# Optimization experiments

Measured on AMD Instinct MI355X. Metric: run time of the kernel, lower is better.

The kernel has to match this reference:

```python
import jax, jax.numpy as jnp
import numpy as np

B, T, LE = 8, 128, 128
V, VEXT = 32000, 32100
D, H, DFF, MAXLEN = 512, 8, 2048, 512


def _ln(x, g, b, eps=1e-5):
    m = jnp.mean(x, axis=-1, keepdims=True)
    v = jnp.mean((x - m) ** 2, axis=-1, keepdims=True)
    return (x - m) / jnp.sqrt(v + eps) * g + b


def _mha(q_in, k_in, v_in, in_w, in_b, out_w, out_b, mask=None):
    # torch nn.MultiheadAttention (batch_first): packed in_proj [3D, D]
    d = q_in.shape[-1]
    dh = d // H
    wq, wk, wv = in_w[:d], in_w[d:2 * d], in_w[2 * d:]
    bq, bk, bv = in_b[:d], in_b[d:2 * d], in_b[2 * d:]
    q = q_in @ wq.T + bq
    k = k_in @ wk.T + bk
    v = v_in @ wv.T + bv
    def split(x):  # [B, L, D] -> [B, H, L, dh]
        b, l, _ = x.shape
        return x.reshape(b, l, H, dh).transpose(0, 2, 1, 3)
    q, k, v = split(q), split(k), split(v)
    scores = jnp.einsum('bhqd,bhkd->bhqk', q, k) / jnp.sqrt(jnp.asarray(dh, q.dtype))
    if mask is not None:
        scores = scores + mask  # broadcast [T, T] additive mask
    attn = jax.nn.softmax(scores, axis=-1)  # [B, H, Lq, Lk]
    out = jnp.einsum('bhqk,bhkd->bhqd', attn, v)
    b, _, lq, _ = out.shape
    out = out.transpose(0, 2, 1, 3).reshape(b, lq, d)
    return out @ out_w.T + out_b, attn


def setup_inputs() -> dict:
    key = jax.random.key(0)
    ks = jax.random.split(key, 16)
    s = 0.02
    p = lambda i, shape: jax.random.normal(ks[i], shape, jnp.float32) * s
    return {
        'trg_input_ids': jax.random.randint(ks[0], (B, T), 0, V),
        'emofused': jax.random.normal(ks[1], (B, LE, D), jnp.float32),
        'src_token_ids': jax.random.randint(ks[2], (B, LE), 0, VEXT),
        'extended_vocab_size': VEXT,
        'tok_emb': p(3, (V, D)),
        'pos_emb': p(4, (MAXLEN, D)),
        'sa_in_w': p(5, (3 * D, D)), 'sa_in_b': jnp.zeros(3 * D, jnp.float32),
        'sa_out_w': p(6, (D, D)), 'sa_out_b': jnp.zeros(D, jnp.float32),
        'ca_in_w': p(7, (3 * D, D)), 'ca_in_b': jnp.zeros(3 * D, jnp.float32),
        'ca_out_w': p(8, (D, D)), 'ca_out_b': jnp.zeros(D, jnp.float32),
        'w1': p(9, (DFF, D)), 'b1': jnp.zeros(DFF, jnp.float32),
        'w2': p(10, (D, DFF)), 'b2': jnp.zeros(D, jnp.float32),
        'n1_g': jnp.ones(D, jnp.float32), 'n1_b': jnp.zeros(D, jnp.float32),
        'n2_g': jnp.ones(D, jnp.float32), 'n2_b': jnp.zeros(D, jnp.float32),
        'n3_g': jnp.ones(D, jnp.float32), 'n3_b': jnp.zeros(D, jnp.float32),
        'vp_w': p(11, (V, D)), 'vp_b': jnp.zeros(V, jnp.float32),
        'pg_w': p(12, (1, 3 * D)), 'pg_b': jnp.zeros(1, jnp.float32),
    }


def reference(trg_input_ids, emofused, src_token_ids, extended_vocab_size,
              tok_emb, pos_emb, sa_in_w, sa_in_b, sa_out_w, sa_out_b,
              ca_in_w, ca_in_b, ca_out_w, ca_out_b, w1, b1, w2, b2,
              n1_g, n1_b, n2_g, n2_b, n3_g, n3_b, vp_w, vp_b, pg_w, pg_b):
    t = trg_input_ids.shape[1]
    emb = tok_emb[trg_input_ids]                      # [B, T, D]
    x = emb + pos_emb[:t][None]
    # causal additive mask [T, T]
    idx = jnp.arange(t)
    mask = jnp.where(idx[None, :] > idx[:, None], jnp.asarray(-1e9, x.dtype), 0.0)
    # pre-norm self-attn
    h = _ln(x, n1_g, n1_b)
    sa, _ = _mha(h, h, h, sa_in_w, sa_in_b, sa_out_w, sa_out_b, mask)
    x = x + sa
    # pre-norm cross-attn (emofused is sole KV)
    h = _ln(x, n2_g, n2_b)
    ca, ca_attn = _mha(h, emofused, emofused, ca_in_w, ca_in_b, ca_out_w, ca_out_b)
    x = x + ca
    # FFN
    h = _ln(x, n3_g, n3_b)
    x = x + (jax.nn.relu(h @ w1.T + b1) @ w2.T + b2)
    hidden = x
    attn_avg = ca_attn.mean(axis=1)                   # [B, T, LE]
    ctx = jnp.einsum('btl,bld->btd', attn_avg, emofused)
    Pgen = jax.nn.softmax(hidden @ vp_w.T + vp_b, axis=-1)  # [B, T, V]
    gate_in = jnp.concatenate([hidden, ctx, emb], axis=-1)
    p_mix = jax.nn.sigmoid(gate_in @ pg_w.T + pg_b)   # [B, T, 1]
    vext = int(extended_vocab_size)
    def scat(aw, src):  # aw [T, LE], src [LE] -> [T, Vext]
        return jnp.zeros((aw.shape[0], vext), aw.dtype).at[:, src].add(aw)
    Pcopy = jax.vmap(scat)(attn_avg, src_token_ids)   # [B, T, Vext]
    Pgen_ext = jnp.pad(Pgen, ((0, 0), (0, 0), (0, vext - Pgen.shape[-1])))
    Pw = p_mix * Pgen_ext + (1.0 - p_mix) * Pcopy
    return Pw, Pgen_ext, Pcopy, p_mix, hidden, attn_avg, ctx
```

## Files before the change

kernel.cpp:

```cpp
#include <hip/hip_runtime.h>
#include <hip/hip_bf16.h>

using bf16   = __hip_bfloat16;
using bf16x8 = __attribute__((ext_vector_type(8))) __bf16;
using f32x4  = __attribute__((ext_vector_type(4))) float;
using short8 = __attribute__((ext_vector_type(8))) short;

__device__ __forceinline__ unsigned short f2b(float x) {
  union { bf16 b; unsigned short u; } t; t.b = __float2bfloat16(x); return t.u;
}
__device__ __forceinline__ float b2f(unsigned short u) {
  union { unsigned int i; float f; } t; t.i = ((unsigned int)u) << 16; return t.f;
}
__device__ __forceinline__ void ntst4(float* p, float a, float b, float c, float d) {
  f32x4 v = {a, b, c, d};
  __builtin_nontemporal_store(v, (f32x4*)p);
}

typedef __attribute__((address_space(1))) const unsigned int* gas1_t;
typedef __attribute__((address_space(3))) unsigned int* las3_t;
__device__ __forceinline__ void gload16(const void* g, void* l) {
  __builtin_amdgcn_global_load_lds((gas1_t)g, (las3_t)l, 16, 0, 0);
}

__global__ __launch_bounds__(256) void k_cast_all(
    const float* __restrict__ vpsrc, bf16* __restrict__ vpdst,
    const float* __restrict__ s0, bf16* __restrict__ d0,
    const float* __restrict__ s1, bf16* __restrict__ d1,
    const float* __restrict__ s2, bf16* __restrict__ d2,
    const float* __restrict__ s3, bf16* __restrict__ d3,
    const float* __restrict__ s4, bf16* __restrict__ d4,
    const float* __restrict__ s5, bf16* __restrict__ d5,
    const float* __restrict__ s6, bf16* __restrict__ d6,
    float* __restrict__ rowsum) {
  int i = blockIdx.x * 256 + threadIdx.x;
  int str = gridDim.x * 256;
  for (; i < 5275904; i += str) {
    if (i < 4096000) {
      float4 v = ((const float4*)vpsrc)[i];
      ushort4 u; u.x = f2b(v.x); u.y = f2b(v.y); u.z = f2b(v.z); u.w = f2b(v.w);
      ((ushort4*)vpdst)[i] = u;
    } else if (i < 5275648) {
      int j = i - 4096000;
      const float* s; bf16* d; int off;
      if      (j <  196608) { s = s0; d = d0; off = j; }
      else if (j <  262144) { s = s1; d = d1; off = j - 196608; }
      else if (j <  458752) { s = s2; d = d2; off = j - 262144; }
      else if (j <  524288) { s = s3; d = d3; off = j - 458752; }
      else if (j <  786432) { s = s4; d = d4; off = j - 524288; }
      else if (j < 1048576) { s = s5; d = d5; off = j - 786432; }
      else                  { s = s6; d = d6; off = j - 1048576; }
      float4 v = ((const float4*)s)[off];
      ushort4 u; u.x = f2b(v.x); u.y = f2b(v.y); u.z = f2b(v.z); u.w = f2b(v.w);
      ((ushort4*)d)[off] = u;
    } else {
      float4 z = {0.f, 0.f, 0.f, 0.f};
      ((float4*)rowsum)[i - 5275648] = z;
    }
  }
}

__global__ __launch_bounds__(256) void k_embed_ln(const int* __restrict__ ids, const float* __restrict__ tok,
                                                  const float* __restrict__ pos, const float* __restrict__ g,
                                                  const float* __restrict__ bb, float* __restrict__ x,
                                                  float* __restrict__ emb, bf16* __restrict__ o) {
  int wid = threadIdx.x >> 6, lane = threadIdx.x & 63;
  int row = blockIdx.x * 4 + wid;
  int tt = row & 127;
  int id = ids[row];
  int d = lane * 8;
  float4 e0 = *(const float4*)&tok[(size_t)id * 512 + d];
  float4 e1 = *(const float4*)&tok[(size_t)id * 512 + d + 4];
  float4 p0 = *(const float4*)&pos[(size_t)tt * 512 + d];
  float4 p1 = *(const float4*)&pos[(size_t)tt * 512 + d + 4];
  *(float4*)&emb[(size_t)row * 512 + d]     = e0;
  *(float4*)&emb[(size_t)row * 512 + d + 4] = e1;
  float4 v0; v0.x = e0.x + p0.x; v0.y = e0.y + p0.y; v0.z = e0.z + p0.z; v0.w = e0.w + p0.w;
  float4 v1; v1.x = e1.x + p1.x; v1.y = e1.y + p1.y; v1.z = e1.z + p1.z; v1.w = e1.w + p1.w;
  *(float4*)&x[(size_t)row * 512 + d]     = v0;
  *(float4*)&x[(size_t)row * 512 + d + 4] = v1;
  float s = v0.x + v0.y + v0.z + v0.w + v1.x + v1.y + v1.z + v1.w;
  float q = v0.x*v0.x + v0.y*v0.y + v0.z*v0.z + v0.w*v0.w
          + v1.x*v1.x + v1.y*v1.y + v1.z*v1.z + v1.w*v1.w;
#pragma unroll
  for (int t = 32; t; t >>= 1) { s += __shfl_xor(s, t); q += __shfl_xor(q, t); }
  float mean = s * (1.f / 512.f);
  float var  = q * (1.f / 512.f) - mean * mean;
  float rstd = rsqrtf(var + 1e-5f);
  float4 g0 = *(const float4*)&g[d],  g1 = *(const float4*)&g[d + 4];
  float4 b0 = *(const float4*)&bb[d], b1 = *(const float4*)&bb[d + 4];
  short8 pk;
  pk[0] = (short)f2b((v0.x - mean) * rstd * g0.x + b0.x);
  pk[1] = (short)f2b((v0.y - mean) * rstd * g0.y + b0.y);
  pk[2] = (short)f2b((v0.z - mean) * rstd * g0.z + b0.z);
  pk[3] = (short)f2b((v0.w - mean) * rstd * g0.w + b0.w);
  pk[4] = (short)f2b((v1.x - mean) * rstd * g1.x + b1.x);
  pk[5] = (short)f2b((v1.y - mean) * rstd * g1.y + b1.y);
  pk[6] = (short)f2b((v1.z - mean) * rstd * g1.z + b1.z);
  pk[7] = (short)f2b((v1.w - mean) * rstd * g1.w + b1.w);
  *(short8*)&o[(size_t)row * 512 + d] = pk;
}

__global__ __launch_bounds__(256) void k_ln(const float* __restrict__ x, const float* __restrict__ g,
                                            const float* __restrict__ bb, bf16* __restrict__ o) {
  int wid = threadIdx.x >> 6, lane = threadIdx.x & 63;
  int row = blockIdx.x * 4 + wid;
  const float* xr = x + (size_t)row * 512;
  int d = lane * 8;
  float4 v0 = *(const float4*)&xr[d];
  float4 v1 = *(const float4*)&xr[d + 4];
  float s = v0.x + v0.y + v0.z + v0.w + v1.x + v1.y + v1.z + v1.w;
  float q = v0.x*v0.x + v0.y*v0.y + v0.z*v0.z + v0.w*v0.w
          + v1.x*v1.x + v1.y*v1.y + v1.z*v1.z + v1.w*v1.w;
#pragma unroll
  for (int t = 32; t; t >>= 1) { s += __shfl_xor(s, t); q += __shfl_xor(q, t); }
  float mean = s * (1.f / 512.f);
  float var  = q * (1.f / 512.f) - mean * mean;
  float rstd = rsqrtf(var + 1e-5f);
  float4 g0 = *(const float4*)&g[d],  g1 = *(const float4*)&g[d + 4];
  float4 b0 = *(const float4*)&bb[d], b1 = *(const float4*)&bb[d + 4];
  short8 pk;
  pk[0] = (short)f2b((v0.x - mean) * rstd * g0.x + b0.x);
  pk[1] = (short)f2b((v0.y - mean) * rstd * g0.y + b0.y);
  pk[2] = (short)f2b((v0.z - mean) * rstd * g0.z + b0.z);
  pk[3] = (short)f2b((v0.w - mean) * rstd * g0.w + b0.w);
  pk[4] = (short)f2b((v1.x - mean) * rstd * g1.x + b1.x);
  pk[5] = (short)f2b((v1.y - mean) * rstd * g1.y + b1.y);
  pk[6] = (short)f2b((v1.z - mean) * rstd * g1.z + b1.z);
  pk[7] = (short)f2b((v1.w - mean) * rstd * g1.w + b1.w);
  *(short8*)&o[(size_t)row * 512 + d] = pk;
}

template<int RELU, int RESID, int OUTBF, int SWZ, int HID, int EXPS>
__global__ __launch_bounds__(256) void k_gemm(const bf16* __restrict__ A, const bf16* __restrict__ Wt,
                                              const float* __restrict__ bias, const float* __restrict__ resid,
                                              void* __restrict__ Cout, bf16* __restrict__ hidb,
                                              float* __restrict__ rowsum, int K, int ldc) {
  __shared__ __align__(16) float cst[32 * 132];
  bf16* Al = (bf16*)cst;
  bf16* Bl = (bf16*)cst + 4096;
  int t = threadIdx.x;
  int lane = t & 63;
  int wid = t >> 6;
  int wr = wid >> 1, wc = wid & 1;
  int trow, tcol;
  if (SWZ) {
    int bid = blockIdx.y * gridDim.x + blockIdx.x;
    int swz = (bid & 7) * 250 + (bid >> 3);
    trow = (swz & 7) * 128;
    tcol = (swz >> 3) * 128;
  } else {
    trow = blockIdx.y * 128; tcol = blockIdx.x * 128;
  }
  f32x4 acc[4][4] = {};
  const int kh = (lane >> 4) * 8;
  const int rl = lane & 15;
  const int srow = lane >> 2;
  const int scol = (lane & 3) * 8;
  for (int kt = 0; kt < K; kt += 32) {
    __syncthreads();
#pragma unroll
    for (int s = 0; s < 2; ++s) {
      int c = wid * 2 + s;
      int row = c * 16 + srow;
      gload16(A  + (size_t)(trow + row) * K + kt + scol, &Al[c * 512]);
      gload16(Wt + (size_t)(tcol + row) * K + kt + scol, &Bl[c * 512]);
    }
    __syncthreads();
    bf16x8 af[4], bg[4];
#pragma unroll
    for (int m = 0; m < 4; ++m) af[m] = *(const bf16x8*)&Al[(wr * 64 + m * 16 + rl) * 32 + kh];
#pragma unroll
    for (int n = 0; n < 4; ++n) bg[n] = *(const bf16x8*)&Bl[(wc * 64 + n * 16 + rl) * 32 + kh];
#pragma unroll
    for (int m = 0; m < 4; ++m)
#pragma unroll
      for (int n = 0; n < 4; ++n)
        acc[m][n] = __builtin_amdgcn_mfma_f32_16x16x32_bf16(af[m], bg[n], acc[m][n], 0, 0, 0);
  }
  const int s   = t >> 3;
  const int seg = (t & 7) * 16;
  float bv[16];
#pragma unroll
  for (int q = 0; q < 16; q += 4) *(float4*)&bv[q] = *(const float4*)&bias[tcol + seg + q];
#pragma unroll
  for (int m = 0; m < 4; ++m) {
    __syncthreads();
#pragma unroll
    for (int n = 0; n < 4; ++n) {
      int col = wc * 64 + n * 16 + rl;
#pragma unroll
      for (int j = 0; j < 4; ++j) {
        int sr = wr * 16 + (lane >> 4) * 4 + j;
        cst[sr * 132 + col] = acc[m][n][j];
      }
    }
    __syncthreads();
    int grow = trow + m * 16 + (s < 16 ? s : 48 + s);
    size_t base = (size_t)grow * ldc + tcol + seg;
    float v[16];
#pragma unroll
    for (int q = 0; q < 16; q += 4) {
      float4 f = *(float4*)&cst[s * 132 + seg + q];
      v[q] = f.x; v[q+1] = f.y; v[q+2] = f.z; v[q+3] = f.w;
    }
    if (RESID) {
#pragma unroll
      for (int q = 0; q < 16; q += 4) {
        float4 r = *(const float4*)&resid[base + q];
        v[q] += r.x; v[q+1] += r.y; v[q+2] += r.z; v[q+3] += r.w;
      }
    }
#pragma unroll
    for (int q = 0; q < 16; ++q) {
      float val = v[q] + bv[q];
      if (RELU) val = fmaxf(val, 0.f);
      v[q] = val;
    }
    if (OUTBF) {
      short8 p0, p1;
#pragma unroll
      for (int q = 0; q < 8; ++q) { p0[q] = (short)f2b(v[q]); p1[q] = (short)f2b(v[8 + q]); }
      *(short8*)&((bf16*)Cout)[base]     = p0;
      *(short8*)&((bf16*)Cout)[base + 8] = p1;
      if (EXPS) {
        float e = 0.f;
#pragma unroll
        for (int q = 0; q < 8; ++q)
          e += __expf(b2f((unsigned short)p0[q])) + __expf(b2f((unsigned short)p1[q]));
        e += __shfl_xor(e, 1); e += __shfl_xor(e, 2); e += __shfl_xor(e, 4);
        if ((t & 7) == 0) atomicAdd(&rowsum[grow], e);
      }
    } else {
#pragma unroll
      for (int q = 0; q < 16; q += 4) {
        float4 o; o.x = v[q]; o.y = v[q+1]; o.z = v[q+2]; o.w = v[q+3];
        *(float4*)&((float*)Cout)[base + q] = o;
      }
      if (HID) {
        short8 p0, p1;
#pragma unroll
        for (int q = 0; q < 8; ++q) { p0[q] = (short)f2b(v[q]); p1[q] = (short)f2b(v[8 + q]); }
        *(short8*)&hidb[base]     = p0;
        *(short8*)&hidb[base + 8] = p1;
      }
    }
  }
}

template<int MASK, int WPROB>
__global__ __launch_bounds__(256) void k_attn(const float* __restrict__ Qb, int qs,
                                              const float* __restrict__ Kb, int ks,
                                              const float* __restrict__ Vb, int vs,
                                              float* __restrict__ probs, bf16* __restrict__ Ob, int os) {
  __shared__ float KV[128][68];
  __shared__ float Sc[32][132];
  int t = threadIdx.x;
  int bh = blockIdx.x; int b = bh >> 3, h = bh & 7;
  int rb = blockIdx.y * 32;
  int r = t >> 3, sub = t & 7;
  const float* Kp = Kb + (size_t)(b * 128) * ks + h * 64;
  const float* Vp = Vb + (size_t)(b * 128) * vs + h * 64;
  const float* Qp = Qb + (size_t)(b * 128 + rb + r) * qs + h * 64;
  float4 q[16];
#pragma unroll
  for (int i = 0; i < 16; ++i) q[i] = *(const float4*)&Qp[i * 4];
  for (int i = 0; i < 32; ++i) { int u = t + i * 256; int rr = u >> 6, dd = u & 63; KV[rr][dd] = Kp[(size_t)rr * ks + dd]; }
  __syncthreads();
  float sc[16];
#pragma unroll
  for (int i = 0; i < 16; ++i) {
    int c = sub + i * 8;
    float a = 0.f;
#pragma unroll
    for (int d4 = 0; d4 < 16; ++d4) {
      float4 k4 = *(const float4*)&KV[c][d4 * 4];
      a += q[d4].x * k4.x + q[d4].y * k4.y + q[d4].z * k4.z + q[d4].w * k4.w;
    }
    a *= 0.125f;
    if (MASK && c > rb + r) a -= 1e9f;
    sc[i] = a;
  }
  float mx = -1e30f;
#pragma unroll
  for (int i = 0; i < 16; ++i) mx = fmaxf(mx, sc[i]);
  mx = fmaxf(mx, __shfl_xor(mx, 1)); mx = fmaxf(mx, __shfl_xor(mx, 2)); mx = fmaxf(mx, __shfl_xor(mx, 4));
  float sm = 0.f;
#pragma unroll
  for (int i = 0; i < 16; ++i) { sc[i] = __expf(sc[i] - mx); sm += sc[i]; }
  sm += __shfl_xor(sm, 1); sm += __shfl_xor(sm, 2); sm += __shfl_xor(sm, 4);
  float inv = 1.f / sm;
#pragma unroll
  for (int i = 0; i < 16; ++i) {
    float p = sc[i] * inv;
    Sc[r][sub + i * 8] = p;
    if (WPROB) probs[(((size_t)(b * 8 + h) * 128) + rb + r) * 128 + sub + i * 8] = p;
  }
  __syncthreads();
  for (int i = 0; i < 32; ++i) { int u = t + i * 256; int rr = u >> 6, dd = u & 63; KV[rr][dd] = Vp[(size_t)rr * vs + dd]; }
  __syncthreads();
  int dg = sub;
  float4 o0 = {0,0,0,0}, o1 = {0,0,0,0};
  for (int j = 0; j < 128; ++j) {
    float p = Sc[r][j];
    float4 va = *(const float4*)&KV[j][dg * 8];
    float4 vb = *(const float4*)&KV[j][dg * 8 + 4];
    o0.x += p * va.x; o0.y += p * va.y; o0.z += p * va.z; o0.w += p * va.w;
    o1.x += p * vb.x; o1.y += p * vb.y; o1.z += p * vb.z; o1.w += p * vb.w;
  }
  short8 pk;
  pk[0] = (short)f2b(o0.x); pk[1] = (short)f2b(o0.y); pk[2] = (short)f2b(o0.z); pk[3] = (short)f2b(o0.w);
  pk[4] = (short)f2b(o1.x); pk[5] = (short)f2b(o1.y); pk[6] = (short)f2b(o1.z); pk[7] = (short)f2b(o1.w);
  *(short8*)&Ob[(size_t)(b * 128 + rb + r) * os + h * 64 + dg * 8] = pk;
}

__global__ __launch_bounds__(256) void k_ctx2(const float* __restrict__ abuf, const float* __restrict__ emo,
                                              float* __restrict__ aavg, float* __restrict__ ctx) {
  __shared__ float aw[8][132];
  int b = blockIdx.x, rb = blockIdx.y * 8;
  int t = threadIdx.x;
  for (int i = t; i < 1024; i += 256) {
    int r = i >> 7, l = i & 127;
    float s = 0.f;
#pragma unroll
    for (int h = 0; h < 8; ++h) s += abuf[(((size_t)(b * 8 + h) * 128) + rb + r) * 128 + l];
    s *= 0.125f;
    aw[r][l] = s;
    aavg[(size_t)(b * 128 + rb + r) * 128 + l] = s;
  }
  __syncthreads();
  int d = t * 2;
  float2 acc[8] = {};
  for (int l = 0; l < 128; ++l) {
    float2 e = *(const float2*)&emo[(size_t)(b * 128 + l) * 512 + d];
#pragma unroll
    for (int r = 0; r < 8; ++r) { acc[r].x += aw[r][l] * e.x; acc[r].y += aw[r][l] * e.y; }
  }
#pragma unroll
  for (int r = 0; r < 8; ++r) *(float2*)&ctx[(size_t)(b * 128 + rb + r) * 512 + d] = acc[r];
}

__global__ __launch_bounds__(256) void k_softmax_final(
    const bf16* __restrict__ lg, const float* __restrict__ rowsum,
    const float* __restrict__ hid, const float* __restrict__ ctx, const float* __restrict__ emb,
    const float* __restrict__ pgw, const float* __restrict__ pgb,
    float* __restrict__ pmix_out, float* __restrict__ pgen, float* __restrict__ pw,
    float* __restrict__ pcopy) {
  __shared__ float red[4];
  int row = blockIdx.x;
  int t = threadIdx.x, lane = t & 63, wid = t >> 6;
  float s;
  {
    int d = t * 2;
    float2 h2 = *(const float2*)&hid[(size_t)row * 512 + d];
    float2 c2 = *(const float2*)&ctx[(size_t)row * 512 + d];
    float2 e2 = *(const float2*)&emb[(size_t)row * 512 + d];
    float2 g0 = *(const float2*)&pgw[d];
    float2 g1 = *(const float2*)&pgw[512 + d];
    float2 g2 = *(const float2*)&pgw[1024 + d];
    s = h2.x*g0.x + h2.y*g0.y + c2.x*g1.x + c2.y*g1.y + e2.x*g2.x + e2.y*g2.y;
  }
#pragma unroll
  for (int o = 32; o; o >>= 1) s += __shfl_xor(s, o);
  if (lane == 0) red[wid] = s;
  __syncthreads();
  s = red[0] + red[1] + red[2] + red[3];
  float pm = 1.f / (1.f + __expf(-(s + pgb[0])));
  if (t == 0) pmix_out[row] = pm;
  float inv = 1.f / rowsum[row];
  const bf16* L = lg + (size_t)row * 32000;
  float* pgen_r  = pgen  + (size_t)row * 32100;
  float* pw_r    = pw    + (size_t)row * 32100;
  float* pcopy_r = pcopy + (size_t)row * 32100;
  for (int i = t; i < 4000; i += 256) {
    short8 v = *(const short8*)(L + i * 8);
    float p[8];
#pragma unroll
    for (int c = 0; c < 8; ++c) p[c] = __expf(b2f((unsigned short)v[c])) * inv;
    ntst4(&pgen_r[i * 8],     p[0], p[1], p[2], p[3]);
    ntst4(&pgen_r[i * 8 + 4], p[4], p[5], p[6], p[7]);
    ntst4(&pw_r[i * 8],     pm * p[0], pm * p[1], pm * p[2], pm * p[3]);
    ntst4(&pw_r[i * 8 + 4], pm * p[4], pm * p[5], pm * p[6], pm * p[7]);
    ntst4(&pcopy_r[i * 8],     0.f, 0.f, 0.f, 0.f);
    ntst4(&pcopy_r[i * 8 + 4], 0.f, 0.f, 0.f, 0.f);
  }
  if (t < 25) {
    int c = 32000 + t * 4;
    ntst4(&pgen_r[c], 0.f, 0.f, 0.f, 0.f);
    ntst4(&pw_r[c],   0.f, 0.f, 0.f, 0.f);
    ntst4(&pcopy_r[c], 0.f, 0.f, 0.f, 0.f);
  }
}

__global__ __launch_bounds__(256) void k_scatter(const int* __restrict__ src, const float* __restrict__ aavg,
                                                 const float* __restrict__ pmix, float* __restrict__ pw,
                                                 float* __restrict__ pcopy) {
  int tid = blockIdx.x * 256 + threadIdx.x;
  int row = tid >> 4, slot = tid & 15;
  int b = row >> 7;
  float qg = 1.f - pmix[row];
#pragma unroll
  for (int i = 0; i < 8; ++i) {
    int l = slot * 8 + i;
    int c = src[b * 128 + l];
    float w = aavg[(size_t)row * 128 + l];
    atomicAdd(&pcopy[(size_t)row * 32100 + c], w);
    atomicAdd(&pw[(size_t)row * 32100 + c], qg * w);
  }
}

extern "C" void kernel_launch(void* const* d_in, const int* in_sizes, int n_in,
                              void* d_out, int out_size, void* d_ws, size_t ws_size,
                              hipStream_t stream) {
  const int*   ids      = (const int*)d_in[0];
  const float* emo      = (const float*)d_in[1];
  const int*   src      = (const int*)d_in[2];
  const float* tok      = (const float*)d_in[4];
  const float* pos      = (const float*)d_in[5];
  const float* sa_in_w  = (const float*)d_in[6];
  const float* sa_in_b  = (const float*)d_in[7];
  const float* sa_out_w = (const float*)d_in[8];
  const float* sa_out_b = (const float*)d_in[9];
  const float* ca_in_w  = (const float*)d_in[10];
  const float* ca_in_b  = (const float*)d_in[11];
  const float* ca_out_w = (const float*)d_in[12];
  const float* ca_out_b = (const float*)d_in[13];
  const float* w1       = (const float*)d_in[14];
  const float* b1       = (const float*)d_in[15];
  const float* w2       = (const float*)d_in[16];
  const float* b2       = (const float*)d_in[17];
  const float* n1g      = (const float*)d_in[18];
  const float* n1b      = (const float*)d_in[19];
  const float* n2g      = (const float*)d_in[20];
  const float* n2b      = (const float*)d_in[21];
  const float* n3g      = (const float*)d_in[22];
  const float* n3b      = (const float*)d_in[23];
  const float* vpw      = (const float*)d_in[24];
  const float* vpb      = (const float*)d_in[25];
  const float* pgw      = (const float*)d_in[26];
  const float* pgb      = (const float*)d_in[27];
  (void)in_sizes; (void)n_in; (void)out_size; (void)ws_size;

  constexpr size_t NR = 1024;
  float* out     = (float*)d_out;
  float* o_pw    = out;
  float* o_pgen  = out + NR * 32100;
  float* o_pcopy = out + 2 * NR * 32100;
  float* o_pmix  = out + 3 * NR * 32100;
  float* o_hid   = o_pmix + NR;
  float* o_aavg  = o_hid + NR * 512;
  float* o_ctx   = o_aavg + NR * 128;

  char* wp = (char*)d_ws;
  size_t off = 0;
  auto alloc = [&](size_t bytes) { char* r = wp + off; off += (bytes + 255) & ~(size_t)255; return r; };
  bf16*  sa_in_bf  = (bf16*)alloc(3 * 512 * 512 * 2);
  bf16*  sa_out_bf = (bf16*)alloc(512 * 512 * 2);
  bf16*  ca_in_bf  = (bf16*)alloc(3 * 512 * 512 * 2);
  bf16*  ca_out_bf = (bf16*)alloc(512 * 512 * 2);
  bf16*  w1_bf     = (bf16*)alloc(2048 * 512 * 2);
  bf16*  w2_bf     = (bf16*)alloc(2048 * 512 * 2);
  bf16*  vp_bf     = (bf16*)alloc((size_t)32000 * 512 * 2);
  bf16*  emo_bf    = (bf16*)alloc(8 * 128 * 512 * 2);
  float* x         = (float*)alloc(1024 * 512 * 4);
  float* embf      = (float*)alloc(1024 * 512 * 4);
  bf16*  hbf       = (bf16*)alloc(1024 * 512 * 2);
  float* qkv       = (float*)alloc(1024 * 1536 * 4);
  bf16*  aout_bf   = (bf16*)alloc(1024 * 512 * 2);
  float* qca       = (float*)alloc(1024 * 512 * 4);
  float* kvca      = (float*)alloc(1024 * 1024 * 4);
  float* abuf      = (float*)alloc((size_t)8 * 8 * 128 * 128 * 4);
  bf16*  f1bf      = (bf16*)alloc(1024 * 2048 * 2);
  bf16*  hid_bf    = (bf16*)alloc(1024 * 512 * 2);
  bf16*  logits_bf = (bf16*)alloc((size_t)1024 * 32000 * 2);
  float* rowsum    = (float*)alloc(1024 * 4);

  k_cast_all<<<4608, 256, 0, stream>>>(vpw, vp_bf,
                                       sa_in_w, sa_in_bf, sa_out_w, sa_out_bf,
                                       ca_in_w, ca_in_bf, ca_out_w, ca_out_bf,
                                       w1, w1_bf, w2, w2_bf, emo, emo_bf, rowsum);

  k_embed_ln<<<256, 256, 0, stream>>>(ids, tok, pos, n1g, n1b, x, embf, hbf);

  k_gemm<0,0,0,0,0,0><<<dim3(12, 8), 256, 0, stream>>>(hbf, sa_in_bf, sa_in_b, nullptr, qkv, nullptr, nullptr, 512, 1536);
  k_attn<1,0><<<dim3(64, 4), 256, 0, stream>>>(qkv, 1536, qkv + 512, 1536, qkv + 1024, 1536,
                                               nullptr, aout_bf, 512);
  k_gemm<0,1,0,0,0,0><<<dim3(4, 8), 256, 0, stream>>>(aout_bf, sa_out_bf, sa_out_b, x, x, nullptr, nullptr, 512, 512);

  k_ln<<<256, 256, 0, stream>>>(x, n2g, n2b, hbf);
  k_gemm<0,0,0,0,0,0><<<dim3(4, 8), 256, 0, stream>>>(hbf, ca_in_bf, ca_in_b, nullptr, qca, nullptr, nullptr, 512, 512);
  k_gemm<0,0,0,0,0,0><<<dim3(8, 8), 256, 0, stream>>>(emo_bf, ca_in_bf + 512 * 512, ca_in_b + 512,
                                                      nullptr, kvca, nullptr, nullptr, 512, 1024);
  k_attn<0,1><<<dim3(64, 4), 256, 0, stream>>>(qca, 512, kvca, 1024, kvca + 512, 1024,
                                               abuf, aout_bf, 512);
  k_ctx2<<<dim3(8, 16), 256, 0, stream>>>(abuf, emo, o_aavg, o_ctx);
  k_gemm<0,1,0,0,0,0><<<dim3(4, 8), 256, 0, stream>>>(aout_bf, ca_out_bf, ca_out_b, x, x, nullptr, nullptr, 512, 512);

  k_ln<<<256, 256, 0, stream>>>(x, n3g, n3b, hbf);
  k_gemm<1,0,1,0,0,0><<<dim3(16, 8), 256, 0, stream>>>(hbf, w1_bf, b1, nullptr, f1bf, nullptr, nullptr, 512, 2048);
  k_gemm<0,1,0,0,1,0><<<dim3(4, 8), 256, 0, stream>>>(f1bf, w2_bf, b2, x, o_hid, hid_bf, nullptr, 2048, 512);

  k_gemm<0,0,1,1,0,1><<<dim3(8, 250), 256, 0, stream>>>(hid_bf, vp_bf, vpb, nullptr, logits_bf, nullptr, rowsum, 512, 32000);

  k_softmax_final<<<1024, 256, 0, stream>>>(logits_bf, rowsum, o_hid, o_ctx, embf, pgw, pgb,
                                            o_pmix, o_pgen, o_pw, o_pcopy);

  k_scatter<<<64, 256, 0, stream>>>(src, o_aavg, o_pmix, o_pw, o_pcopy);
}
```

Measured before the change: 464.3 us.

## Fuse fp32 vocab-weight cast into vocab GEMM and use per-tile partial sums

The separate bf16 cast of the 32000x512 vocab projection weight is removed. The new vocab GEMM loads the fp32 weights directly into swizzled LDS and converts them to bf16 while forming MFMA fragments. This avoids a full weight read/write round trip, but the GEMM now streams twice the weight bytes and spends extra ALU on conversion. The atomic rowsum accumulation is replaced by a per-column-tile partial buffer that the softmax kernel reduces, which also removes the rowsum zeroing. Nontemporal stores in the final softmax are changed to plain stores.

```diff
diff --git a/kernel.cpp b/kernel.cpp
--- a/kernel.cpp
+++ b/kernel.cpp
@@ -12,10 +12,6 @@
 __device__ __forceinline__ float b2f(unsigned short u) {
   union { unsigned int i; float f; } t; t.i = ((unsigned int)u) << 16; return t.f;
 }
-__device__ __forceinline__ void ntst4(float* p, float a, float b, float c, float d) {
-  f32x4 v = {a, b, c, d};
-  __builtin_nontemporal_store(v, (f32x4*)p);
-}
 
 typedef __attribute__((address_space(1))) const unsigned int* gas1_t;
 typedef __attribute__((address_space(3))) unsigned int* las3_t;
@@ -24,39 +20,28 @@
 }
 
 __global__ __launch_bounds__(256) void k_cast_all(
-    const float* __restrict__ vpsrc, bf16* __restrict__ vpdst,
     const float* __restrict__ s0, bf16* __restrict__ d0,
     const float* __restrict__ s1, bf16* __restrict__ d1,
     const float* __restrict__ s2, bf16* __restrict__ d2,
     const float* __restrict__ s3, bf16* __restrict__ d3,
     const float* __restrict__ s4, bf16* __restrict__ d4,
     const float* __restrict__ s5, bf16* __restrict__ d5,
-    const float* __restrict__ s6, bf16* __restrict__ d6,
-    float* __restrict__ rowsum) {
+    const float* __restrict__ s6, bf16* __restrict__ d6) {
   int i = blockIdx.x * 256 + threadIdx.x;
   int str = gridDim.x * 256;
-  for (; i < 5275904; i += str) {
-    if (i < 4096000) {
-      float4 v = ((const float4*)vpsrc)[i];
-      ushort4 u; u.x = f2b(v.x); u.y = f2b(v.y); u.z = f2b(v.z); u.w = f2b(v.w);
-      ((ushort4*)vpdst)[i] = u;
-    } else if (i < 5275648) {
-      int j = i - 4096000;
-      const float* s; bf16* d; int off;
-      if      (j <  196608) { s = s0; d = d0; off = j; }
-      else if (j <  262144) { s = s1; d = d1; off = j - 196608; }
-      else if (j <  458752) { s = s2; d = d2; off = j - 262144; }
-      else if (j <  524288) { s = s3; d = d3; off = j - 458752; }
-      else if (j <  786432) { s = s4; d = d4; off = j - 524288; }
-      else if (j < 1048576) { s = s5; d = d5; off = j - 786432; }
-      else                  { s = s6; d = d6; off = j - 1048576; }
-      float4 v = ((const float4*)s)[off];
-      ushort4 u; u.x = f2b(v.x); u.y = f2b(v.y); u.z = f2b(v.z); u.w = f2b(v.w);
-      ((ushort4*)d)[off] = u;
-    } else {
-      float4 z = {0.f, 0.f, 0.f, 0.f};
-      ((float4*)rowsum)[i - 5275648] = z;
-    }
+  for (; i < 1179648; i += str) {
+    int j = i;
+    const float* s; bf16* d; int off;
+    if      (j <  196608) { s = s0; d = d0; off = j; }
+    else if (j <  262144) { s = s1; d = d1; off = j - 196608; }
+    else if (j <  458752) { s = s2; d = d2; off = j - 262144; }
+    else if (j <  524288) { s = s3; d = d3; off = j - 458752; }
+    else if (j <  786432) { s = s4; d = d4; off = j - 524288; }
+    else if (j < 1048576) { s = s5; d = d5; off = j - 786432; }
+    else                  { s = s6; d = d6; off = j - 1048576; }
+    float4 v = ((const float4*)s)[off];
+    ushort4 u; u.x = f2b(v.x); u.y = f2b(v.y); u.z = f2b(v.z); u.w = f2b(v.w);
+    ((ushort4*)d)[off] = u;
   }
 }
 
@@ -131,11 +116,11 @@
   *(short8*)&o[(size_t)row * 512 + d] = pk;
 }
 
-template<int RELU, int RESID, int OUTBF, int SWZ, int HID, int EXPS>
+template<int RELU, int RESID, int OUTBF, int HID>
 __global__ __launch_bounds__(256) void k_gemm(const bf16* __restrict__ A, const bf16* __restrict__ Wt,
                                               const float* __restrict__ bias, const float* __restrict__ resid,
                                               void* __restrict__ Cout, bf16* __restrict__ hidb,
-                                              float* __restrict__ rowsum, int K, int ldc) {
+                                              int K, int ldc) {
   __shared__ __align__(16) float cst[32 * 132];
   bf16* Al = (bf16*)cst;
   bf16* Bl = (bf16*)cst + 4096;
@@ -143,15 +128,7 @@
   int lane = t & 63;
   int wid = t >> 6;
   int wr = wid >> 1, wc = wid & 1;
-  int trow, tcol;
-  if (SWZ) {
-    int bid = blockIdx.y * gridDim.x + blockIdx.x;
-    int swz = (bid & 7) * 250 + (bid >> 3);
-    trow = (swz & 7) * 128;
-    tcol = (swz >> 3) * 128;
-  } else {
-    trow = blockIdx.y * 128; tcol = blockIdx.x * 128;
-  }
+  int trow = blockIdx.y * 128, tcol = blockIdx.x * 128;
   f32x4 acc[4][4] = {};
   const int kh = (lane >> 4) * 8;
   const int rl = lane & 15;
@@ -223,14 +200,6 @@
       for (int q = 0; q < 8; ++q) { p0[q] = (short)f2b(v[q]); p1[q] = (short)f2b(v[8 + q]); }
       *(short8*)&((bf16*)Cout)[base]     = p0;
       *(short8*)&((bf16*)Cout)[base + 8] = p1;
-      if (EXPS) {
-        float e = 0.f;
-#pragma unroll
-        for (int q = 0; q < 8; ++q)
-          e += __expf(b2f((unsigned short)p0[q])) + __expf(b2f((unsigned short)p1[q]));
-        e += __shfl_xor(e, 1); e += __shfl_xor(e, 2); e += __shfl_xor(e, 4);
-        if ((t & 7) == 0) atomicAdd(&rowsum[grow], e);
-      }
     } else {
 #pragma unroll
       for (int q = 0; q < 16; q += 4) {
@@ -245,6 +214,104 @@
         *(short8*)&hidb[base + 8] = p1;
       }
     }
+  }
+}
+
+__global__ __launch_bounds__(256) void k_gemm_vp(const bf16* __restrict__ A, const float* __restrict__ Wt,
+                                                 const float* __restrict__ bias, bf16* __restrict__ Cout,
+                                                 float* __restrict__ partial, int K, int ldc) {
+  __shared__ __align__(16) float cst[6144];
+  bf16*  Al = (bf16*)cst;
+  float* Bl = cst + 2048;
+  int t = threadIdx.x;
+  int lane = t & 63;
+  int wid = t >> 6;
+  int wr = wid >> 1, wc = wid & 1;
+  int bid = blockIdx.y * gridDim.x + blockIdx.x;
+  int swz = (bid & 7) * 250 + (bid >> 3);
+  int trow = (swz & 7) * 128;
+  int ct   = swz >> 3;
+  int tcol = ct * 128;
+  f32x4 acc[4][4] = {};
+  const int kh = (lane >> 4) * 8;
+  const int rl = lane & 15;
+  const int srow = lane >> 2;
+  const int scol = (lane & 3) * 8;
+  for (int kt = 0; kt < K; kt += 32) {
+    __syncthreads();
+#pragma unroll
+    for (int s = 0; s < 2; ++s) {
+      int c = wid * 2 + s;
+      int row = c * 16 + srow;
+      gload16(A + (size_t)(trow + row) * K + kt + scol, &Al[c * 512]);
+    }
+#pragma unroll
+    for (int s = 0; s < 4; ++s) {
+      int li  = s * 256 + t;
+      int row = li >> 3;
+      int cb  = (li & 7) * 16;
+      int sc  = cb ^ ((row & 7) << 4);
+      gload16(Wt + (size_t)(tcol + row) * K + kt + (sc >> 2), &Bl[s * 1024 + wid * 256]);
+    }
+    __syncthreads();
+    bf16x8 af[4], bg[4];
+#pragma unroll
+    for (int m = 0; m < 4; ++m) af[m] = *(const bf16x8*)&Al[(wr * 64 + m * 16 + rl) * 32 + kh];
+#pragma unroll
+    for (int n = 0; n < 4; ++n) {
+      int row = wc * 64 + n * 16 + rl;
+      int rx  = (row & 7) << 4;
+      const char* bp = (const char*)(Bl + row * 32);
+      float4 x0 = *(const float4*)(bp + ((kh * 4) ^ rx));
+      float4 x1 = *(const float4*)(bp + ((kh * 4 + 16) ^ rx));
+      short8 tb;
+      tb[0] = (short)f2b(x0.x); tb[1] = (short)f2b(x0.y); tb[2] = (short)f2b(x0.z); tb[3] = (short)f2b(x0.w);
+      tb[4] = (short)f2b(x1.x); tb[5] = (short)f2b(x1.y); tb[6] = (short)f2b(x1.z); tb[7] = (short)f2b(x1.w);
+      bg[n] = __builtin_bit_cast(bf16x8, tb);
+    }
+#pragma unroll
+    for (int m = 0; m < 4; ++m)
+#pragma unroll
+      for (int n = 0; n < 4; ++n)
+        acc[m][n] = __builtin_amdgcn_mfma_f32_16x16x32_bf16(af[m], bg[n], acc[m][n], 0, 0, 0);
+  }
+  const int s   = t >> 3;
+  const int seg = (t & 7) * 16;
+  float bv[16];
+#pragma unroll
+  for (int q = 0; q < 16; q += 4) *(float4*)&bv[q] = *(const float4*)&bias[tcol + seg + q];
+#pragma unroll
+  for (int m = 0; m < 4; ++m) {
+    __syncthreads();
+#pragma unroll
+    for (int n = 0; n < 4; ++n) {
+      int col = wc * 64 + n * 16 + rl;
+#pragma unroll
+      for (int j = 0; j < 4; ++j)
+        cst[(wr * 16 + (lane >> 4) * 4 + j) * 132 + col] = acc[m][n][j];
+    }
+    __syncthreads();
+    int grow = trow + m * 16 + (s < 16 ? s : 48 + s);
+    size_t base = (size_t)grow * ldc + tcol + seg;
+    float v[16];
+#pragma unroll
+    for (int q = 0; q < 16; q += 4) {
+      float4 f = *(float4*)&cst[s * 132 + seg + q];
+      v[q] = f.x; v[q+1] = f.y; v[q+2] = f.z; v[q+3] = f.w;
+    }
+    short8 p0, p1;
+    float e = 0.f;
+#pragma unroll
+    for (int q = 0; q < 8; ++q) {
+      unsigned short u0 = f2b(v[q] + bv[q]);
+      unsigned short u1 = f2b(v[8 + q] + bv[8 + q]);
+      p0[q] = (short)u0; p1[q] = (short)u1;
+      e += __expf(b2f(u0)) + __expf(b2f(u1));
+    }
+    *(short8*)&Cout[base]     = p0;
+    *(short8*)&Cout[base + 8] = p1;
+    e += __shfl_xor(e, 1); e += __shfl_xor(e, 2); e += __shfl_xor(e, 4);
+    if ((t & 7) == 0) partial[(size_t)grow * 256 + ct] = e;
   }
 }
 
@@ -341,12 +408,12 @@
 }
 
 __global__ __launch_bounds__(256) void k_softmax_final(
-    const bf16* __restrict__ lg, const float* __restrict__ rowsum,
+    const bf16* __restrict__ lg, const float* __restrict__ partial,
     const float* __restrict__ hid, const float* __restrict__ ctx, const float* __restrict__ emb,
     const float* __restrict__ pgw, const float* __restrict__ pgb,
     float* __restrict__ pmix_out, float* __restrict__ pgen, float* __restrict__ pw,
     float* __restrict__ pcopy) {
-  __shared__ float red[4];
+  __shared__ float red[8];
   int row = blockIdx.x;
   int t = threadIdx.x, lane = t & 63, wid = t >> 6;
   float s;
@@ -360,35 +427,40 @@
     float2 g2 = *(const float2*)&pgw[1024 + d];
     s = h2.x*g0.x + h2.y*g0.y + c2.x*g1.x + c2.y*g1.y + e2.x*g2.x + e2.y*g2.y;
   }
-#pragma unroll
-  for (int o = 32; o; o >>= 1) s += __shfl_xor(s, o);
-  if (lane == 0) red[wid] = s;
+  float rs = (t < 250) ? partial[(size_t)row * 256 + t] : 0.f;
+#pragma unroll
+  for (int o = 32; o; o >>= 1) { s += __shfl_xor(s, o); rs += __shfl_xor(rs, o); }
+  if (lane == 0) { red[wid] = s; red[4 + wid] = rs; }
   __syncthreads();
-  s = red[0] + red[1] + red[2] + red[3];
+  s  = red[0] + red[1] + red[2] + red[3];
+  rs = red[4] + red[5] + red[6] + red[7];
   float pm = 1.f / (1.f + __expf(-(s + pgb[0])));
   if (t == 0) pmix_out[row] = pm;
-  float inv = 1.f / rowsum[row];
+  float inv = 1.f / rs;
   const bf16* L = lg + (size_t)row * 32000;
   float* pgen_r  = pgen  + (size_t)row * 32100;
   float* pw_r    = pw    + (size_t)row * 32100;
   float* pcopy_r = pcopy + (size_t)row * 32100;
+  float4 z = {0.f, 0.f, 0.f, 0.f};
   for (int i = t; i < 4000; i += 256) {
     short8 v = *(const short8*)(L + i * 8);
     float p[8];
 #pragma unroll
     for (int c = 0; c < 8; ++c) p[c] = __expf(b2f((unsigned short)v[c])) * inv;
-    ntst4(&pgen_r[i * 8],     p[0], p[1], p[2], p[3]);
-    ntst4(&pgen_r[i * 8 + 4], p[4], p[5], p[6], p[7]);
-    ntst4(&pw_r[i * 8],     pm * p[0], pm * p[1], pm * p[2], pm * p[3]);
-    ntst4(&pw_r[i * 8 + 4], pm * p[4], pm * p[5], pm * p[6], pm * p[7]);
-    ntst4(&pcopy_r[i * 8],     0.f, 0.f, 0.f, 0.f);
-    ntst4(&pcopy_r[i * 8 + 4], 0.f, 0.f, 0.f, 0.f);
+    float4 a0 = {p[0], p[1], p[2], p[3]};
+    float4 a1 = {p[4], p[5], p[6], p[7]};
+    *(float4*)&pgen_r[i * 8]     = a0;
+    *(float4*)&pgen_r[i * 8 + 4] = a1;
+    float4 w0 = {pm * p[0], pm * p[1], pm * p[2], pm * p[3]};
+    float4 w1 = {pm * p[4], pm * p[5], pm * p[6], pm * p[7]};
+    *(float4*)&pw_r[i * 8]     = w0;
+    *(float4*)&pw_r[i * 8 + 4] = w1;
+    *(float4*)&pcopy_r[i * 8]     = z;
+    *(float4*)&pcopy_r[i * 8 + 4] = z;
   }
   if (t < 25) {
     int c = 32000 + t * 4;
-    ntst4(&pgen_r[c], 0.f, 0.f, 0.f, 0.f);
-    ntst4(&pw_r[c],   0.f, 0.f, 0.f, 0.f);
-    ntst4(&pcopy_r[c], 0.f, 0.f, 0.f, 0.f);
+    *(float4*)&pgen_r[c] = z; *(float4*)&pw_r[c] = z; *(float4*)&pcopy_r[c] = z;
   }
 }
 
@@ -460,7 +532,6 @@
   bf16*  ca_out_bf = (bf16*)alloc(512 * 512 * 2);
   bf16*  w1_bf     = (bf16*)alloc(2048 * 512 * 2);
   bf16*  w2_bf     = (bf16*)alloc(2048 * 512 * 2);
-  bf16*  vp_bf     = (bf16*)alloc((size_t)32000 * 512 * 2);
   bf16*  emo_bf    = (bf16*)alloc(8 * 128 * 512 * 2);
   float* x         = (float*)alloc(1024 * 512 * 4);
   float* embf      = (float*)alloc(1024 * 512 * 4);
@@ -473,36 +544,35 @@
   bf16*  f1bf      = (bf16*)alloc(1024 * 2048 * 2);
   bf16*  hid_bf    = (bf16*)alloc(1024 * 512 * 2);
   bf16*  logits_bf = (bf16*)alloc((size_t)1024 * 32000 * 2);
-  float* rowsum    = (float*)alloc(1024 * 4);
-
-  k_cast_all<<<4608, 256, 0, stream>>>(vpw, vp_bf,
-                                       sa_in_w, sa_in_bf, sa_out_w, sa_out_bf,
+  float* partial   = (float*)alloc((size_t)1024 * 256 * 4);
+
+  k_cast_all<<<2048, 256, 0, stream>>>(sa_in_w, sa_in_bf, sa_out_w, sa_out_bf,
                                        ca_in_w, ca_in_bf, ca_out_w, ca_out_bf,
-                                       w1, w1_bf, w2, w2_bf, emo, emo_bf, rowsum);
+                                       w1, w1_bf, w2, w2_bf, emo, emo_bf);
 
   k_embed_ln<<<256, 256, 0, stream>>>(ids, tok, pos, n1g, n1b, x, embf, hbf);
 
-  k_gemm<0,0,0,0,0,0><<<dim3(12, 8), 256, 0, stream>>>(hbf, sa_in_bf, sa_in_b, nullptr, qkv, nullptr, nullptr, 512, 1536);
+  k_gemm<0,0,0,0><<<dim3(12, 8), 256, 0, stream>>>(hbf, sa_in_bf, sa_in_b, nullptr, qkv, nullptr, 512, 1536);
   k_attn<1,0><<<dim3(64, 4), 256, 0, stream>>>(qkv, 1536, qkv + 512, 1536, qkv + 1024, 1536,
                                                nullptr, aout_bf, 512);
-  k_gemm<0,1,0,0,0,0><<<dim3(4, 8), 256, 0, stream>>>(aout_bf, sa_out_bf, sa_out_b, x, x, nullptr, nullptr, 512, 512);
+  k_gemm<0,1,0,0><<<dim3(4, 8), 256, 0, stream>>>(aout_bf, sa_out_bf, sa_out_b, x, x, nullptr, 512, 512);
 
   k_ln<<<256, 256, 0, stream>>>(x, n2g, n2b, hbf);
-  k_gemm<0,0,0,0,0,0><<<dim3(4, 8), 256, 0, stream>>>(hbf, ca_in_bf, ca_in_b, nullptr, qca, nullptr, nullptr, 512, 512);
-  k_gemm<0,0,0,0,0,0><<<dim3(8, 8), 256, 0, stream>>>(emo_bf, ca_in_bf + 512 * 512, ca_in_b + 512,
-                                                      nullptr, kvca, nullptr, nullptr, 512, 1024);
+  k_gemm<0,0,0,0><<<dim3(4, 8), 256, 0, stream>>>(hbf, ca_in_bf, ca_in_b, nullptr, qca, nullptr, 512, 512);
+  k_gemm<0,0,0,0><<<dim3(8, 8), 256, 0, stream>>>(emo_bf, ca_in_bf + 512 * 512, ca_in_b + 512,
+                                                  nullptr, kvca, nullptr, 512, 1024);
   k_attn<0,1><<<dim3(64, 4), 256, 0, stream>>>(qca, 512, kvca, 1024, kvca + 512, 1024,
                                                abuf, aout_bf, 512);
   k_ctx2<<<dim3(8, 16), 256, 0, stream>>>(abuf, emo, o_aavg, o_ctx);
-  k_gemm<0,1,0,0,0,0><<<dim3(4, 8), 256, 0, stream>>>(aout_bf, ca_out_bf, ca_out_b, x, x, nullptr, nullptr, 512, 512);
+  k_gemm<0,1,0,0><<<dim3(4, 8), 256, 0, stream>>>(aout_bf, ca_out_bf, ca_out_b, x, x, nullptr, 512, 512);
 
   k_ln<<<256, 256, 0, stream>>>(x, n3g, n3b, hbf);
-  k_gemm<1,0,1,0,0,0><<<dim3(16, 8), 256, 0, stream>>>(hbf, w1_bf, b1, nullptr, f1bf, nullptr, nullptr, 512, 2048);
-  k_gemm<0,1,0,0,1,0><<<dim3(4, 8), 256, 0, stream>>>(f1bf, w2_bf, b2, x, o_hid, hid_bf, nullptr, 2048, 512);
-
-  k_gemm<0,0,1,1,0,1><<<dim3(8, 250), 256, 0, stream>>>(hid_bf, vp_bf, vpb, nullptr, logits_bf, nullptr, rowsum, 512, 32000);
-
-  k_softmax_final<<<1024, 256, 0, stream>>>(logits_bf, rowsum, o_hid, o_ctx, embf, pgw, pgb,
+  k_gemm<1,0,1,0><<<dim3(16, 8), 256, 0, stream>>>(hbf, w1_bf, b1, nullptr, f1bf, nullptr, 512, 2048);
+  k_gemm<0,1,0,1><<<dim3(4, 8), 256, 0, stream>>>(f1bf, w2_bf, b2, x, o_hid, hid_bf, 2048, 512);
+
+  k_gemm_vp<<<dim3(8, 250), 256, 0, stream>>>(hid_bf, vpw, vpb, logits_bf, partial, 512, 32000);
+
+  k_softmax_final<<<1024, 256, 0, stream>>>(logits_bf, partial, o_hid, o_ctx, embf, pgw, pgb,
                                             o_pmix, o_pgen, o_pw, o_pcopy);
 
   k_scatter<<<64, 256, 0, stream>>>(src, o_aavg, o_pmix, o_pw, o_pcopy);
```

After: 469.4 us. About the same (+1.1%).

## Replace softmax rowsum atomics with per-tile partial sums; use normal stores

Applied to the files above, without the earlier changes.

The vocab GEMM now writes each 128-column tile's exp-sum into a per-row partial buffer instead of issuing atomicAdds to a shared rowsum. The softmax kernel reduces the 250 partials itself, so the zeroing pass in the cast kernel goes away. The large output stores switch from nontemporal to regular float4 stores. This removes atomic contention but adds a small partial buffer and an extra reduction. Regular stores may pollute the cache on the roughly 400MB of output writes.

```diff
diff --git a/kernel.cpp b/kernel.cpp
--- a/kernel.cpp
+++ b/kernel.cpp
@@ -11,10 +11,6 @@
 }
 __device__ __forceinline__ float b2f(unsigned short u) {
   union { unsigned int i; float f; } t; t.i = ((unsigned int)u) << 16; return t.f;
-}
-__device__ __forceinline__ void ntst4(float* p, float a, float b, float c, float d) {
-  f32x4 v = {a, b, c, d};
-  __builtin_nontemporal_store(v, (f32x4*)p);
 }
 
 typedef __attribute__((address_space(1))) const unsigned int* gas1_t;
@@ -31,16 +27,15 @@
     const float* __restrict__ s3, bf16* __restrict__ d3,
     const float* __restrict__ s4, bf16* __restrict__ d4,
     const float* __restrict__ s5, bf16* __restrict__ d5,
-    const float* __restrict__ s6, bf16* __restrict__ d6,
-    float* __restrict__ rowsum) {
+    const float* __restrict__ s6, bf16* __restrict__ d6) {
   int i = blockIdx.x * 256 + threadIdx.x;
   int str = gridDim.x * 256;
-  for (; i < 5275904; i += str) {
+  for (; i < 5275648; i += str) {
     if (i < 4096000) {
       float4 v = ((const float4*)vpsrc)[i];
       ushort4 u; u.x = f2b(v.x); u.y = f2b(v.y); u.z = f2b(v.z); u.w = f2b(v.w);
       ((ushort4*)vpdst)[i] = u;
-    } else if (i < 5275648) {
+    } else {
       int j = i - 4096000;
       const float* s; bf16* d; int off;
       if      (j <  196608) { s = s0; d = d0; off = j; }
@@ -53,9 +48,6 @@
       float4 v = ((const float4*)s)[off];
       ushort4 u; u.x = f2b(v.x); u.y = f2b(v.y); u.z = f2b(v.z); u.w = f2b(v.w);
       ((ushort4*)d)[off] = u;
-    } else {
-      float4 z = {0.f, 0.f, 0.f, 0.f};
-      ((float4*)rowsum)[i - 5275648] = z;
     }
   }
 }
@@ -135,7 +127,7 @@
 __global__ __launch_bounds__(256) void k_gemm(const bf16* __restrict__ A, const bf16* __restrict__ Wt,
                                               const float* __restrict__ bias, const float* __restrict__ resid,
                                               void* __restrict__ Cout, bf16* __restrict__ hidb,
-                                              float* __restrict__ rowsum, int K, int ldc) {
+                                              float* __restrict__ partial, int K, int ldc) {
   __shared__ __align__(16) float cst[32 * 132];
   bf16* Al = (bf16*)cst;
   bf16* Bl = (bf16*)cst + 4096;
@@ -229,7 +221,7 @@
         for (int q = 0; q < 8; ++q)
           e += __expf(b2f((unsigned short)p0[q])) + __expf(b2f((unsigned short)p1[q]));
         e += __shfl_xor(e, 1); e += __shfl_xor(e, 2); e += __shfl_xor(e, 4);
-        if ((t & 7) == 0) atomicAdd(&rowsum[grow], e);
+        if ((t & 7) == 0) partial[(size_t)grow * 256 + (tcol >> 7)] = e;
       }
     } else {
 #pragma unroll
@@ -341,12 +333,12 @@
 }
 
 __global__ __launch_bounds__(256) void k_softmax_final(
-    const bf16* __restrict__ lg, const float* __restrict__ rowsum,
+    const bf16* __restrict__ lg, const float* __restrict__ partial,
     const float* __restrict__ hid, const float* __restrict__ ctx, const float* __restrict__ emb,
     const float* __restrict__ pgw, const float* __restrict__ pgb,
     float* __restrict__ pmix_out, float* __restrict__ pgen, float* __restrict__ pw,
     float* __restrict__ pcopy) {
-  __shared__ float red[4];
+  __shared__ float red[8];
   int row = blockIdx.x;
   int t = threadIdx.x, lane = t & 63, wid = t >> 6;
   float s;
@@ -360,35 +352,40 @@
     float2 g2 = *(const float2*)&pgw[1024 + d];
     s = h2.x*g0.x + h2.y*g0.y + c2.x*g1.x + c2.y*g1.y + e2.x*g2.x + e2.y*g2.y;
   }
-#pragma unroll
-  for (int o = 32; o; o >>= 1) s += __shfl_xor(s, o);
-  if (lane == 0) red[wid] = s;
+  float rs = (t < 250) ? partial[(size_t)row * 256 + t] : 0.f;
+#pragma unroll
+  for (int o = 32; o; o >>= 1) { s += __shfl_xor(s, o); rs += __shfl_xor(rs, o); }
+  if (lane == 0) { red[wid] = s; red[4 + wid] = rs; }
   __syncthreads();
-  s = red[0] + red[1] + red[2] + red[3];
+  s  = red[0] + red[1] + red[2] + red[3];
+  rs = red[4] + red[5] + red[6] + red[7];
   float pm = 1.f / (1.f + __expf(-(s + pgb[0])));
   if (t == 0) pmix_out[row] = pm;
-  float inv = 1.f / rowsum[row];
+  float inv = 1.f / rs;
   const bf16* L = lg + (size_t)row * 32000;
   float* pgen_r  = pgen  + (size_t)row * 32100;
   float* pw_r    = pw    + (size_t)row * 32100;
   float* pcopy_r = pcopy + (size_t)row * 32100;
+  float4 z = {0.f, 0.f, 0.f, 0.f};
   for (int i = t; i < 4000; i += 256) {
     short8 v = *(const short8*)(L + i * 8);
     float p[8];
 #pragma unroll
     for (int c = 0; c < 8; ++c) p[c] = __expf(b2f((unsigned short)v[c])) * inv;
-    ntst4(&pgen_r[i * 8],     p[0], p[1], p[2], p[3]);
-    ntst4(&pgen_r[i * 8 + 4], p[4], p[5], p[6], p[7]);
-    ntst4(&pw_r[i * 8],     pm * p[0], pm * p[1], pm * p[2], pm * p[3]);
-    ntst4(&pw_r[i * 8 + 4], pm * p[4], pm * p[5], pm * p[6], pm * p[7]);
-    ntst4(&pcopy_r[i * 8],     0.f, 0.f, 0.f, 0.f);
-    ntst4(&pcopy_r[i * 8 + 4], 0.f, 0.f, 0.f, 0.f);
+    float4 a0 = {p[0], p[1], p[2], p[3]};
+    float4 a1 = {p[4], p[5], p[6], p[7]};
+    *(float4*)&pgen_r[i * 8]     = a0;
+    *(float4*)&pgen_r[i * 8 + 4] = a1;
+    float4 w0 = {pm * p[0], pm * p[1], pm * p[2], pm * p[3]};
+    float4 w1 = {pm * p[4], pm * p[5], pm * p[6], pm * p[7]};
+    *(float4*)&pw_r[i * 8]     = w0;
+    *(float4*)&pw_r[i * 8 + 4] = w1;
+    *(float4*)&pcopy_r[i * 8]     = z;
+    *(float4*)&pcopy_r[i * 8 + 4] = z;
   }
   if (t < 25) {
     int c = 32000 + t * 4;
-    ntst4(&pgen_r[c], 0.f, 0.f, 0.f, 0.f);
-    ntst4(&pw_r[c],   0.f, 0.f, 0.f, 0.f);
-    ntst4(&pcopy_r[c], 0.f, 0.f, 0.f, 0.f);
+    *(float4*)&pgen_r[c] = z; *(float4*)&pw_r[c] = z; *(float4*)&pcopy_r[c] = z;
   }
 }
 
@@ -473,12 +470,12 @@
   bf16*  f1bf      = (bf16*)alloc(1024 * 2048 * 2);
   bf16*  hid_bf    = (bf16*)alloc(1024 * 512 * 2);
   bf16*  logits_bf = (bf16*)alloc((size_t)1024 * 32000 * 2);
-  float* rowsum    = (float*)alloc(1024 * 4);
+  float* partial   = (float*)alloc((size_t)1024 * 256 * 4);
 
   k_cast_all<<<4608, 256, 0, stream>>>(vpw, vp_bf,
                                        sa_in_w, sa_in_bf, sa_out_w, sa_out_bf,
                                        ca_in_w, ca_in_bf, ca_out_w, ca_out_bf,
-                                       w1, w1_bf, w2, w2_bf, emo, emo_bf, rowsum);
+                                       w1, w1_bf, w2, w2_bf, emo, emo_bf);
 
   k_embed_ln<<<256, 256, 0, stream>>>(ids, tok, pos, n1g, n1b, x, embf, hbf);
 
@@ -500,9 +497,9 @@
   k_gemm<1,0,1,0,0,0><<<dim3(16, 8), 256, 0, stream>>>(hbf, w1_bf, b1, nullptr, f1bf, nullptr, nullptr, 512, 2048);
   k_gemm<0,1,0,0,1,0><<<dim3(4, 8), 256, 0, stream>>>(f1bf, w2_bf, b2, x, o_hid, hid_bf, nullptr, 2048, 512);
 
-  k_gemm<0,0,1,1,0,1><<<dim3(8, 250), 256, 0, stream>>>(hid_bf, vp_bf, vpb, nullptr, logits_bf, nullptr, rowsum, 512, 32000);
-
-  k_softmax_final<<<1024, 256, 0, stream>>>(logits_bf, rowsum, o_hid, o_ctx, embf, pgw, pgb,
+  k_gemm<0,0,1,1,0,1><<<dim3(8, 250), 256, 0, stream>>>(hid_bf, vp_bf, vpb, nullptr, logits_bf, nullptr, partial, 512, 32000);
+
+  k_softmax_final<<<1024, 256, 0, stream>>>(logits_bf, partial, o_hid, o_ctx, embf, pgw, pgb,
                                             o_pmix, o_pgen, o_pw, o_pcopy);
 
   k_scatter<<<64, 256, 0, stream>>>(src, o_aavg, o_pmix, o_pw, o_pcopy);
```

Result: faster. 453.5 us (-2.3%).
